# Kernel optimization log

Hardware: AMD Instinct MI355X
Metric: run time of the kernel (lower is better)

## Reference

```python
import jax, jax.numpy as jnp
import numpy as np

D_MODEL = 1024
B, T = 4, 2048
NEG = -1000000000.0


def setup_inputs() -> dict:
    key = jax.random.key(0)
    kq, kk, kv = jax.random.split(key, 3)
    query = jax.random.normal(kq, (B, T, D_MODEL), dtype=jnp.float32)
    k = jax.random.normal(kk, (B, T, D_MODEL), dtype=jnp.float32)
    value = jax.random.normal(kv, (B, T, D_MODEL), dtype=jnp.float32)
    # causal mask: 1.0 where attention is disallowed (strictly upper triangular)
    mask = jnp.triu(jnp.ones((T, T), dtype=jnp.float32), k=1)
    return {"query": query, "key": k, "value": value, "mask": mask}


def reference(query, key, value, mask):
    # dk = sqrt(1/d_model); logits = QK^T / dk  (i.e. * sqrt(d_model)) -- faithful to source
    dk = jnp.sqrt(jnp.float32(1.0) / jnp.float32(D_MODEL))
    attn_logits = jnp.einsum("btc,bsc->bts", query, key) / dk
    attn_logits = attn_logits + mask * NEG  # mask broadcasts over batch
    score = jax.nn.softmax(attn_logits, axis=-1)
    attention = jnp.einsum("bts,bsc->btc", score, value)
    return attention
```

## Files before the change

### kernel.cpp

```cpp
#include <hip/hip_runtime.h>

#define BB 4
#define TT 2048
#define DD 1024
#define SCALE 32.0f
#define NTILE 136
#define L2E 1.4426950408889634f

typedef _Float16 f16;
typedef __attribute__((ext_vector_type(4))) _Float16 half4v;
typedef __attribute__((ext_vector_type(8))) _Float16 half8v;
typedef __attribute__((ext_vector_type(16))) float f32x16;

typedef const __attribute__((address_space(1))) unsigned int* gas_u32;
typedef __attribute__((address_space(3))) unsigned int* las_u32;

static __device__ inline void gload16(const void* g, void* l) {
    __builtin_amdgcn_global_load_lds((gas_u32)g, (las_u32)l, 16, 0, 0);
}

static __device__ inline half8v ld_frag(const f16* p) {
    half4v a = *(const half4v*)p;
    half4v b = *(const half4v*)(p + 4);
    half8v r;
    r[0] = a[0]; r[1] = a[1]; r[2] = a[2]; r[3] = a[3];
    r[4] = b[0]; r[5] = b[1]; r[6] = b[2]; r[7] = b[3];
    return r;
}


__global__ __launch_bounds__(256) void repack_qk(const float* __restrict__ Q,
                                                 const float* __restrict__ K,
                                                 f16* __restrict__ Qt,
                                                 f16* __restrict__ Kt) {
    const int total = 2 * BB * TT * (DD / 8);
    for (int gid = blockIdx.x * 256 + threadIdx.x; gid < total; gid += gridDim.x * 256) {
        int g = gid & 127;
        int t = (gid >> 7) & 2047;
        int b = (gid >> 18) & 3;
        int which = gid >> 20;
        const float* src = which ? K : Q;
        f16* dst = which ? Kt : Qt;
        float sc = which ? 1.0f : SCALE;
        const float* p = src + ((size_t)(b * TT + t)) * DD + g * 8;
        float4 x0 = *(const float4*)p;
        float4 x1 = *(const float4*)(p + 4);
        float vv[8] = {x0.x, x0.y, x0.z, x0.w, x1.x, x1.y, x1.z, x1.w};
        half8v hi, lo;
#pragma unroll
        for (int e = 0; e < 8; ++e) {
            float x = vv[e] * sc;
            f16 h = (f16)x;
            hi[e] = h;
            lo[e] = (f16)(x - (float)h);
        }
        int r = t & 127, mi = t >> 7, ck = g >> 2, gq = g & 3;
        char* base = (char*)dst + ((size_t)((b * 16 + mi) * 32 + ck)) * 16384 + r * 128;
        *(half8v*)(base + ((gq ^ (r & 7)) << 4)) = hi;
        *(half8v*)(base + (((4 + gq) ^ (r & 7)) << 4)) = lo;
    }
}

__global__ __launch_bounds__(256) void transpose_v(const float* __restrict__ V,
                                                   f16* __restrict__ Vt) {
    __shared__ float Vs[64][129];
    int bid = blockIdx.x;
    int b = bid >> 8, kb = (bid >> 3) & 31, nj = bid & 7;
    const float* src = V + ((size_t)(b * TT + kb * 64)) * DD + nj * 128;
    int tid = threadIdx.x;
#pragma unroll
    for (int it = 0; it < 8; ++it) {
        int f4 = it * 256 + tid;
        int row = f4 >> 5, c4 = f4 & 31;
        float4 x = *(const float4*)(src + (size_t)row * DD + c4 * 4);
        Vs[row][c4 * 4 + 0] = x.x;
        Vs[row][c4 * 4 + 1] = x.y;
        Vs[row][c4 * 4 + 2] = x.z;
        Vs[row][c4 * 4 + 3] = x.w;
    }
    __syncthreads();
    char* dbase = (char*)Vt + ((size_t)((b * 8 + nj) * 32 + kb)) * 16384;
#pragma unroll
    for (int it = 0; it < 4; ++it) {
        int gid = it * 256 + tid;
        int n = gid >> 3, s = gid & 7;
        half8v h;
#pragma unroll
        for (int j = 0; j < 8; ++j) h[j] = (f16)Vs[s * 8 + j][n];
        *(half8v*)(dbase + n * 128 + ((s ^ (n & 7)) << 4)) = h;
    }
}

__global__ __launch_bounds__(256, 2) void k1_qk2(const f16* __restrict__ Qt,
                                                 const f16* __restrict__ Kt,
                                                 float* __restrict__ S) {
    __shared__ char lds[65536];

    int bid0 = blockIdx.x;
    int bid = (bid0 & 7) * (BB * NTILE / 8) + (bid0 >> 3);
    int b = bid / NTILE, r = bid % NTILE;
    int mi = 0;
    while ((mi + 1) * (mi + 2) / 2 <= r) ++mi;
    int nj = r - mi * (mi + 1) / 2;

    const char* Abase = (const char*)Qt + ((size_t)((b * 16 + mi) * 32)) * 16384;
    const char* Bbase = (const char*)Kt + ((size_t)((b * 16 + nj) * 32)) * 16384;
    float* Sb = S + (size_t)b * TT * TT + (size_t)(mi * 128) * TT + nj * 128;

    int tid = threadIdx.x;
    int lane = tid & 63;
    int wv = tid >> 6;
    int l31 = lane & 31, lhi = lane >> 5;
    int wrow = wv >> 1, wcol = wv & 1;

    int aoff[2][2], boff[2][2];
#pragma unroll
    for (int fm = 0; fm < 2; ++fm) {
        int ra = wrow * 64 + fm * 32 + l31;
        int rb = wcol * 64 + fm * 32 + l31;
#pragma unroll
        for (int ks = 0; ks < 2; ++ks) {
            int slot = ks * 2 + lhi;
            aoff[fm][ks] = ra * 128 + ((slot ^ (ra & 7)) << 4);
            boff[fm][ks] = rb * 128 + ((slot ^ (rb & 7)) << 4);
        }
    }
    int lane_go = (wv * 256 + lane) * 16;
    int lane_lo = (wv * 256) * 16;

    f32x16 acc[2][2] = {};

#define K1_STAGE(CK, BUF)                                                       \
    {                                                                           \
        const char* ga = Abase + (size_t)(CK) * 16384 + lane_go;                \
        const char* gb = Bbase + (size_t)(CK) * 16384 + lane_go;                \
        char* la = lds + (BUF) * 32768 + lane_lo;                               \
        char* lb = la + 16384;                                                  \
        _Pragma("unroll") for (int i = 0; i < 4; ++i)                           \
            gload16(ga + i * 1024, la + i * 1024);                              \
        _Pragma("unroll") for (int i = 0; i < 4; ++i)                           \
            gload16(gb + i * 1024, lb + i * 1024);                              \
    }

    K1_STAGE(0, 0);
    int cur = 0;
    for (int ck = 0; ck < 32; ++ck) {
        __syncthreads();
        if (ck + 1 < 32) K1_STAGE(ck + 1, cur ^ 1);
        const char* As = lds + cur * 32768;
        const char* Bs = As + 16384;
#pragma unroll
        for (int ks = 0; ks < 2; ++ks) {
            half8v ah[2], al[2], bh[2], bl[2];
#pragma unroll
            for (int f = 0; f < 2; ++f) {
                ah[f] = *(const half8v*)(As + aoff[f][ks]);
                al[f] = *(const half8v*)(As + (aoff[f][ks] ^ 64));
                bh[f] = *(const half8v*)(Bs + boff[f][ks]);
                bl[f] = *(const half8v*)(Bs + (boff[f][ks] ^ 64));
            }
#pragma unroll
            for (int fm = 0; fm < 2; ++fm)
#pragma unroll
                for (int fn = 0; fn < 2; ++fn) {
                    acc[fm][fn] = __builtin_amdgcn_mfma_f32_32x32x16_f16(ah[fm], bh[fn], acc[fm][fn], 0, 0, 0);
                    acc[fm][fn] = __builtin_amdgcn_mfma_f32_32x32x16_f16(ah[fm], bl[fn], acc[fm][fn], 0, 0, 0);
                    acc[fm][fn] = __builtin_amdgcn_mfma_f32_32x32x16_f16(al[fm], bh[fn], acc[fm][fn], 0, 0, 0);
                }
        }
        cur ^= 1;
    }
#pragma unroll
    for (int fm = 0; fm < 2; ++fm)
#pragma unroll
        for (int fn = 0; fn < 2; ++fn)
#pragma unroll
            for (int g = 0; g < 16; ++g) {
                int rr = (g & 3) + 8 * (g >> 2) + 4 * lhi;
                int row = wrow * 64 + fm * 32 + rr;
                int col = wcol * 64 + fn * 32 + l31;
                Sb[(size_t)row * TT + col] = acc[fm][fn][g];
            }
}

__global__ __launch_bounds__(256) void k1b2(const float* __restrict__ S,
                                            f16* __restrict__ Pt) {
    __shared__ float red[4];
    int rowid = blockIdx.x;
    int b = rowid >> 11, t = rowid & (TT - 1);
    const float* Sr = S + ((size_t)b * TT + t) * TT;
    int tid = threadIdx.x;
    int nv = t + 1;
    int mi = t >> 7, r = t & 127;
    int rowend = (mi + 1) << 7;
    int c = tid * 8;

    float4 x0 = *(const float4*)(Sr + c);
    float4 x1 = *(const float4*)(Sr + c + 4);
    float v[8] = {x0.x, x0.y, x0.z, x0.w, x1.x, x1.y, x1.z, x1.w};

    float m = -3.0e38f;
#pragma unroll
    for (int j = 0; j < 8; ++j)
        if (c + j < nv) m = fmaxf(m, v[j]);
#pragma unroll
    for (int o = 32; o > 0; o >>= 1) m = fmaxf(m, __shfl_xor(m, o));
    if ((tid & 63) == 0) red[tid >> 6] = m;
    __syncthreads();
    m = fmaxf(fmaxf(red[0], red[1]), fmaxf(red[2], red[3]));
    __syncthreads();

    float e[8];
    float s = 0.f;
#pragma unroll
    for (int j = 0; j < 8; ++j) {
        e[j] = (c + j < nv) ? exp2f((v[j] - m) * L2E) : 0.0f;
        s += e[j];
    }
#pragma unroll
    for (int o = 32; o > 0; o >>= 1) s += __shfl_xor(s, o);
    if ((tid & 63) == 0) red[tid >> 6] = s;
    __syncthreads();
    s = red[0] + red[1] + red[2] + red[3];
    float inv = 1.0f / s;

    if (c < rowend) {
        half8v h;
#pragma unroll
        for (int j = 0; j < 8; ++j) h[j] = (f16)(e[j] * inv);
        char* dst = (char*)Pt + ((size_t)((b * 16 + mi) * 32 + (c >> 6))) * 16384
                    + r * 128 + ((((c >> 3) & 7) ^ (r & 7)) << 4);
        *(half8v*)dst = h;
    }
}

__global__ __launch_bounds__(256, 2) void k2_pv2(const f16* __restrict__ Pt,
                                                 const f16* __restrict__ Vt,
                                                 float* __restrict__ O) {
    __shared__ char lds[65536];

    int bid0 = blockIdx.x;
    int bid = (bid0 & 7) * (512 / 8) + (bid0 >> 3);
    int b = bid >> 7, mi = (bid >> 3) & 15, nj = bid & 7;
    int kc = (mi + 1) * 2;

    const char* Abase = (const char*)Pt + ((size_t)((b * 16 + mi) * 32)) * 16384;
    const char* Bbase = (const char*)Vt + ((size_t)((b * 8 + nj) * 32)) * 16384;
    float* Ob = O + (size_t)b * TT * DD + (size_t)(mi * 128) * DD + nj * 128;

    int tid = threadIdx.x;
    int lane = tid & 63;
    int wv = tid >> 6;
    int l31 = lane & 31, lhi = lane >> 5;
    int wrow = wv >> 1, wcol = wv & 1;

    int aoff[2][4], boff[2][4];
#pragma unroll
    for (int f = 0; f < 2; ++f) {
        int ra = wrow * 64 + f * 32 + l31;
        int rb = wcol * 64 + f * 32 + l31;
#pragma unroll
        for (int ks = 0; ks < 4; ++ks) {
            int slot = ks * 2 + lhi;
            aoff[f][ks] = ra * 128 + ((slot ^ (ra & 7)) << 4);
            boff[f][ks] = rb * 128 + ((slot ^ (rb & 7)) << 4);
        }
    }
    int lane_go = (wv * 256 + lane) * 16;
    int lane_lo = (wv * 256) * 16;

    f32x16 acc[2][2] = {};

#define K2_STAGE(CK, BUF)                                                       \
    {                                                                           \
        const char* ga = Abase + (size_t)(CK) * 16384 + lane_go;                \
        const char* gb = Bbase + (size_t)(CK) * 16384 + lane_go;                \
        char* la = lds + (BUF) * 32768 + lane_lo;                               \
        char* lb = la + 16384;                                                  \
        _Pragma("unroll") for (int i = 0; i < 4; ++i)                           \
            gload16(ga + i * 1024, la + i * 1024);                              \
        _Pragma("unroll") for (int i = 0; i < 4; ++i)                           \
            gload16(gb + i * 1024, lb + i * 1024);                              \
    }

    K2_STAGE(0, 0);
    int cur = 0;
    for (int ck = 0; ck < kc; ++ck) {
        __syncthreads();
        if (ck + 1 < kc) K2_STAGE(ck + 1, cur ^ 1);
        const char* As = lds + cur * 32768;
        const char* Bs = As + 16384;
#pragma unroll
        for (int ks = 0; ks < 4; ++ks) {
            half8v a0 = *(const half8v*)(As + aoff[0][ks]);
            half8v a1 = *(const half8v*)(As + aoff[1][ks]);
            half8v b0 = *(const half8v*)(Bs + boff[0][ks]);
            half8v b1 = *(const half8v*)(Bs + boff[1][ks]);
            acc[0][0] = __builtin_amdgcn_mfma_f32_32x32x16_f16(a0, b0, acc[0][0], 0, 0, 0);
            acc[0][1] = __builtin_amdgcn_mfma_f32_32x32x16_f16(a0, b1, acc[0][1], 0, 0, 0);
            acc[1][0] = __builtin_amdgcn_mfma_f32_32x32x16_f16(a1, b0, acc[1][0], 0, 0, 0);
            acc[1][1] = __builtin_amdgcn_mfma_f32_32x32x16_f16(a1, b1, acc[1][1], 0, 0, 0);
        }
        cur ^= 1;
    }
#pragma unroll
    for (int fm = 0; fm < 2; ++fm)
#pragma unroll
        for (int fn = 0; fn < 2; ++fn)
#pragma unroll
            for (int g = 0; g < 16; ++g) {
                int rr = (g & 3) + 8 * (g >> 2) + 4 * lhi;
                int row = wrow * 64 + fm * 32 + rr;
                int col = wcol * 64 + fn * 32 + l31;
                Ob[(size_t)row * DD + col] = acc[fm][fn][g];
            }
}

__global__ __launch_bounds__(256, 2) void k1_qk(const float* __restrict__ Q,
                                                const float* __restrict__ Kmat,
                                                float* __restrict__ S) {
    __shared__ f16 Ah[128][36], Al[128][36], Bh[128][36], Bl[128][36];
    int bid = blockIdx.x;
    int b = bid / NTILE, r = bid % NTILE;
    int mi = 0;
    while ((mi + 1) * (mi + 2) / 2 <= r) ++mi;
    int nj = r - mi * (mi + 1) / 2;
    const float* Qb = Q + ((size_t)b * TT + (size_t)mi * 128) * DD;
    const float* Kb = Kmat + ((size_t)b * TT + (size_t)nj * 128) * DD;
    float* Sb = S + (size_t)b * TT * TT + (size_t)(mi * 128) * TT + nj * 128;
    int tid = threadIdx.x;
    int lane = tid & 63;
    int wave = tid >> 6;
    int l31 = lane & 31, lhi = lane >> 5;
    int wrow = wave >> 1, wcol = wave & 1;
    int r0 = tid >> 1;
    int c0 = (tid & 1) * 16;
    f32x16 acc[2][2] = {};
    float4 abuf[4], bbuf[4];
#pragma unroll
    for (int j = 0; j < 4; ++j) {
        abuf[j] = *(const float4*)(Qb + (size_t)r0 * DD + c0 + 4 * j);
        bbuf[j] = *(const float4*)(Kb + (size_t)r0 * DD + c0 + 4 * j);
    }
    for (int ch = 0; ch < DD / 32; ++ch) {
        __syncthreads();
#pragma unroll
        for (int j = 0; j < 4; ++j) {
            float4 a = abuf[j], bq = bbuf[j];
            float ax[4] = {a.x * SCALE, a.y * SCALE, a.z * SCALE, a.w * SCALE};
            float bx[4] = {bq.x, bq.y, bq.z, bq.w};
            half4v ahv, alv, bhv, blv;
#pragma unroll
            for (int e = 0; e < 4; ++e) {
                f16 h = (f16)ax[e];
                ahv[e] = h;
                alv[e] = (f16)(ax[e] - (float)h);
                f16 g = (f16)bx[e];
                bhv[e] = g;
                blv[e] = (f16)(bx[e] - (float)g);
            }
            *(half4v*)&Ah[r0][c0 + 4 * j] = ahv;
            *(half4v*)&Al[r0][c0 + 4 * j] = alv;
            *(half4v*)&Bh[r0][c0 + 4 * j] = bhv;
            *(half4v*)&Bl[r0][c0 + 4 * j] = blv;
        }
        __syncthreads();
        if (ch + 1 < DD / 32) {
            int ck = (ch + 1) * 32;
#pragma unroll
            for (int j = 0; j < 4; ++j) {
                abuf[j] = *(const float4*)(Qb + (size_t)r0 * DD + ck + c0 + 4 * j);
                bbuf[j] = *(const float4*)(Kb + (size_t)r0 * DD + ck + c0 + 4 * j);
            }
        }
#pragma unroll
        for (int ks = 0; ks < 2; ++ks) {
            int kb = ks * 16 + lhi * 8;
            half8v ahf[2], alf[2], bhf[2], blf[2];
#pragma unroll
            for (int f = 0; f < 2; ++f) {
                ahf[f] = ld_frag(&Ah[wrow * 64 + f * 32 + l31][kb]);
                alf[f] = ld_frag(&Al[wrow * 64 + f * 32 + l31][kb]);
                bhf[f] = ld_frag(&Bh[wcol * 64 + f * 32 + l31][kb]);
                blf[f] = ld_frag(&Bl[wcol * 64 + f * 32 + l31][kb]);
            }
#pragma unroll
            for (int fm = 0; fm < 2; ++fm)
#pragma unroll
                for (int fn = 0; fn < 2; ++fn) {
                    acc[fm][fn] = __builtin_amdgcn_mfma_f32_32x32x16_f16(ahf[fm], bhf[fn], acc[fm][fn], 0, 0, 0);
                    acc[fm][fn] = __builtin_amdgcn_mfma_f32_32x32x16_f16(ahf[fm], blf[fn], acc[fm][fn], 0, 0, 0);
                    acc[fm][fn] = __builtin_amdgcn_mfma_f32_32x32x16_f16(alf[fm], bhf[fn], acc[fm][fn], 0, 0, 0);
                }
        }
    }
#pragma unroll
    for (int fm = 0; fm < 2; ++fm)
#pragma unroll
        for (int fn = 0; fn < 2; ++fn)
#pragma unroll
            for (int g = 0; g < 16; ++g) {
                int rr = (g & 3) + 8 * (g >> 2) + 4 * lhi;
                int row = wrow * 64 + fm * 32 + rr;
                int col = wcol * 64 + fn * 32 + l31;
                Sb[(size_t)row * TT + col] = acc[fm][fn][g];
            }
}

__global__ __launch_bounds__(256) void k1b_softmax(const float* __restrict__ S,
                                                   f16* __restrict__ P) {
    __shared__ float red[4];
    int rowid = blockIdx.x;
    int b = rowid >> 11, t = rowid & (TT - 1);
    const float* Sr = S + (size_t)b * TT * TT + (size_t)t * TT;
    f16* Pr = P + (size_t)b * TT * TT + (size_t)t * TT;
    int tid = threadIdx.x;
    int nv = t + 1;
    int rowend = ((t >> 7) + 1) << 7;
    float m = -3.0e38f;
    for (int c = tid; c < nv; c += 256) m = fmaxf(m, Sr[c]);
#pragma unroll
    for (int o = 32; o > 0; o >>= 1) m = fmaxf(m, __shfl_xor(m, o));
    if ((tid & 63) == 0) red[tid >> 6] = m;
    __syncthreads();
    m = fmaxf(fmaxf(red[0], red[1]), fmaxf(red[2], red[3]));
    __syncthreads();
    float s = 0.f;
    for (int c = tid; c < nv; c += 256) s += exp2f((Sr[c] - m) * L2E);
#pragma unroll
    for (int o = 32; o > 0; o >>= 1) s += __shfl_xor(s, o);
    if ((tid & 63) == 0) red[tid >> 6] = s;
    __syncthreads();
    s = red[0] + red[1] + red[2] + red[3];
    float inv = 1.0f / s;
    for (int c = tid; c < rowend; c += 256) {
        float p = (c < nv) ? exp2f((Sr[c] - m) * L2E) * inv : 0.0f;
        Pr[c] = (f16)p;
    }
}

__global__ __launch_bounds__(256, 2) void k2_pv(const f16* __restrict__ P,
                                                const float* __restrict__ V,
                                                float* __restrict__ O) {
    __shared__ f16 Pa[128][36];
    __shared__ f16 Vt[128][36];
    int bid = blockIdx.x;
    int b = bid >> 7;
    int rest = bid & 127;
    int mi = rest >> 3, nj = rest & 7;
    int kend = (mi + 1) * 128;
    const f16* Pb = P + (size_t)b * TT * TT + (size_t)(mi * 128) * TT;
    const float* Vb = V + (size_t)b * TT * DD + nj * 128;
    float* Ob = O + (size_t)b * TT * DD + (size_t)(mi * 128) * DD + nj * 128;
    int tid = threadIdx.x;
    int lane = tid & 63;
    int wave = tid >> 6;
    int l31 = lane & 31, lhi = lane >> 5;
    int wrow = wave >> 1, wcol = wave & 1;
    f32x16 acc[2][2] = {};
    int pr = tid >> 1, pc = (tid & 1) * 16;
    int vk = tid >> 3, vn = (tid & 7) * 16;
    uint2 pbuf[4];
    float4 vbuf[4];
#pragma unroll
    for (int j = 0; j < 4; ++j) {
        pbuf[j] = *(const uint2*)(Pb + (size_t)pr * TT + pc + 4 * j);
        vbuf[j] = *(const float4*)(Vb + (size_t)vk * DD + vn + 4 * j);
    }
    for (int ck = 0; ck < kend; ck += 32) {
        __syncthreads();
#pragma unroll
        for (int j = 0; j < 4; ++j) {
            *(uint2*)&Pa[pr][pc + 4 * j] = pbuf[j];
            float4 v = vbuf[j];
            float vv[4] = {v.x, v.y, v.z, v.w};
            int n0 = vn + 4 * j;
#pragma unroll
            for (int e = 0; e < 4; ++e) {
                int n = n0 + e;
                Vt[n][vk ^ ((((unsigned)n >> 4) & 3) << 3)] = (f16)vv[e];
            }
        }
        __syncthreads();
        if (ck + 32 < kend) {
            int cn = ck + 32;
#pragma unroll
            for (int j = 0; j < 4; ++j) {
                pbuf[j] = *(const uint2*)(Pb + (size_t)pr * TT + cn + pc + 4 * j);
                vbuf[j] = *(const float4*)(Vb + (size_t)(cn + vk) * DD + vn + 4 * j);
            }
        }
#pragma unroll
        for (int ks = 0; ks < 2; ++ks) {
            int kb = ks * 16 + lhi * 8;
            half8v paf[2], vbf[2];
#pragma unroll
            for (int f = 0; f < 2; ++f) {
                paf[f] = ld_frag(&Pa[wrow * 64 + f * 32 + l31][kb]);
                int n = wcol * 64 + f * 32 + l31;
                int kbs = kb ^ ((((unsigned)n >> 4) & 3) << 3);
                vbf[f] = ld_frag(&Vt[n][kbs]);
            }
#pragma unroll
            for (int fm = 0; fm < 2; ++fm)
#pragma unroll
                for (int fn = 0; fn < 2; ++fn)
                    acc[fm][fn] = __builtin_amdgcn_mfma_f32_32x32x16_f16(paf[fm], vbf[fn], acc[fm][fn], 0, 0, 0);
        }
    }
#pragma unroll
    for (int fm = 0; fm < 2; ++fm)
#pragma unroll
        for (int fn = 0; fn < 2; ++fn)
#pragma unroll
            for (int g = 0; g < 16; ++g) {
                int rr = (g & 3) + 8 * (g >> 2) + 4 * lhi;
                int row = wrow * 64 + fm * 32 + rr;
                int col = wcol * 64 + fn * 32 + l31;
                Ob[(size_t)row * DD + col] = acc[fm][fn][g];
            }
}

__global__ __launch_bounds__(256) void fa_fallback(const float* __restrict__ Q,
                                                   const float* __restrict__ Kmat,
                                                   const float* __restrict__ V,
                                                   float* __restrict__ O) {
    __shared__ float qs[DD];
    __shared__ float osum[DD];
    __shared__ float red[4];
    int rowid = blockIdx.x;
    int b = rowid >> 11, t = rowid & (TT - 1);
    const float* q = Q + ((size_t)b * TT + t) * DD;
    int tid = threadIdx.x;
    for (int j = tid; j < DD; j += 256) { qs[j] = q[j] * SCALE; osum[j] = 0.f; }
    __syncthreads();
    float m = -3.0e38f, l = 0.f;
    for (int s = 0; s <= t; ++s) {
        const float* kr = Kmat + ((size_t)b * TT + s) * DD;
        float part = 0.f;
#pragma unroll
        for (int j = 0; j < 4; ++j) part += qs[tid * 4 + j] * kr[tid * 4 + j];
#pragma unroll
        for (int o = 32; o > 0; o >>= 1) part += __shfl_xor(part, o);
        if ((tid & 63) == 0) red[tid >> 6] = part;
        __syncthreads();
        float dot = red[0] + red[1] + red[2] + red[3];
        float mn = fmaxf(m, dot);
        float f = exp2f((m - mn) * 1.44269504f);
        float e = exp2f((dot - mn) * 1.44269504f);
        l = l * f + e;
        const float* vr = V + ((size_t)b * TT + s) * DD;
#pragma unroll
        for (int j = 0; j < 4; ++j) {
            int c = tid * 4 + j;
            osum[c] = osum[c] * f + e * vr[c];
        }
        m = mn;
        __syncthreads();
    }
    float inv = 1.f / l;
    for (int j = tid; j < DD; j += 256) O[((size_t)b * TT + t) * DD + j] = osum[j] * inv;
}

extern "C" void kernel_launch(void* const* d_in, const int* in_sizes, int n_in,
                              void* d_out, int out_size, void* d_ws, size_t ws_size,
                              hipStream_t stream) {
    const float* Q = (const float*)d_in[0];
    const float* K = (const float*)d_in[1];
    const float* V = (const float*)d_in[2];
    float* O = (float*)d_out;

    const size_t MB = 1024 * 1024;
    const size_t QT_B = 32 * MB, KT_B = 32 * MB, VT_B = 16 * MB, S_B = 64 * MB;
    const size_t FULL = QT_B + KT_B + VT_B + S_B;

    size_t sbytes = (size_t)BB * TT * TT * 4;
    size_t pbytes = (size_t)BB * TT * TT * 2;

    if (ws_size >= FULL) {
        f16* Qt = (f16*)d_ws;
        f16* Kt = (f16*)((char*)d_ws + QT_B);
        f16* Vt = (f16*)((char*)d_ws + QT_B + KT_B);
        float* S = (float*)((char*)d_ws + QT_B + KT_B + VT_B);
        f16* Pt = (f16*)d_ws;
        hipLaunchKernelGGL(repack_qk, dim3(2048), dim3(256), 0, stream, Q, K, Qt, Kt);
        hipLaunchKernelGGL(transpose_v, dim3(1024), dim3(256), 0, stream, V, Vt);
        hipLaunchKernelGGL(k1_qk2, dim3(BB * NTILE), dim3(256), 0, stream, Qt, Kt, S);
        hipLaunchKernelGGL(k1b2, dim3(BB * TT), dim3(256), 0, stream, S, Pt);
        hipLaunchKernelGGL(k2_pv2, dim3(512), dim3(256), 0, stream, Pt, Vt, O);
    } else if (ws_size >= sbytes + pbytes) {
        float* S = (float*)d_ws;
        f16* P = (f16*)((char*)d_ws + sbytes);
        hipLaunchKernelGGL(k1_qk, dim3(BB * NTILE), dim3(256), 0, stream, Q, K, S);
        hipLaunchKernelGGL(k1b_softmax, dim3(BB * TT), dim3(256), 0, stream, S, P);
        hipLaunchKernelGGL(k2_pv, dim3(BB * 16 * 8), dim3(256), 0, stream, P, V, O);
    } else {
        hipLaunchKernelGGL(fa_fallback, dim3(BB * TT), dim3(256), 0, stream, Q, K, V, O);
    }
}
```

Before: 153.7 us.

## Switch to slot-major 8KB chunk layout, widen PV tiles, skip masked softmax loads

The repacked Q/K/V/P buffers move from 16KB swizzled chunks to 8KB slot-major chunks, so each fragment row is contiguous and needs no XOR swizzle. QK uses half the LDS per block with occupancy raised to 3, and the PV kernel computes 128x256 output tiles with 256 blocks, reusing each P tile across two V column blocks. Repack_qk now stages through shared memory to write coalesced 128-byte rows, and softmax skips loading S entries beyond the causal tile. The unswizzled LDS layout may cause bank conflicts, and halving the PV grid reduces parallelism on a large GPU.

```diff
diff --git a/kernel.cpp b/kernel.cpp
--- a/kernel.cpp
+++ b/kernel.cpp
@@ -33,32 +33,39 @@
                                                  const float* __restrict__ K,
                                                  f16* __restrict__ Qt,
                                                  f16* __restrict__ Kt) {
-    const int total = 2 * BB * TT * (DD / 8);
-    for (int gid = blockIdx.x * 256 + threadIdx.x; gid < total; gid += gridDim.x * 256) {
-        int g = gid & 127;
-        int t = (gid >> 7) & 2047;
-        int b = (gid >> 18) & 3;
-        int which = gid >> 20;
-        const float* src = which ? K : Q;
-        f16* dst = which ? Kt : Qt;
-        float sc = which ? 1.0f : SCALE;
-        const float* p = src + ((size_t)(b * TT + t)) * DD + g * 8;
-        float4 x0 = *(const float4*)p;
-        float4 x1 = *(const float4*)(p + 4);
+    __shared__ char rl[32768];
+    int bid = blockIdx.x;
+    int which = bid >> 10, b = (bid >> 8) & 3, mi = (bid >> 4) & 15, ks4 = bid & 15;
+    const float* src = which ? K : Q;
+    f16* dst = which ? Kt : Qt;
+    float sc = which ? 1.0f : SCALE;
+
+    int tid = threadIdx.x;
+    int r = tid >> 1, h = tid & 1;
+    const float* p = src + ((size_t)(b * TT + mi * 128 + r)) * DD + ks4 * 64 + h * 32;
+#pragma unroll
+    for (int j = 0; j < 4; ++j) {
+        float4 x0 = *(const float4*)(p + j * 8);
+        float4 x1 = *(const float4*)(p + j * 8 + 4);
         float vv[8] = {x0.x, x0.y, x0.z, x0.w, x1.x, x1.y, x1.z, x1.w};
         half8v hi, lo;
 #pragma unroll
         for (int e = 0; e < 8; ++e) {
             float x = vv[e] * sc;
-            f16 h = (f16)x;
-            hi[e] = h;
-            lo[e] = (f16)(x - (float)h);
-        }
-        int r = t & 127, mi = t >> 7, ck = g >> 2, gq = g & 3;
-        char* base = (char*)dst + ((size_t)((b * 16 + mi) * 32 + ck)) * 16384 + r * 128;
-        *(half8v*)(base + ((gq ^ (r & 7)) << 4)) = hi;
-        *(half8v*)(base + (((4 + gq) ^ (r & 7)) << 4)) = lo;
-    }
+            f16 hh = (f16)x;
+            hi[e] = hh;
+            lo[e] = (f16)(x - (float)hh);
+        }
+        int ckl = h * 2 + (j >> 1);
+        int shalf = j & 1;
+        *(half8v*)(rl + ckl * 8192 + shalf * 2048 + r * 16) = hi;
+        *(half8v*)(rl + ckl * 8192 + (2 + shalf) * 2048 + r * 16) = lo;
+    }
+    __syncthreads();
+    char* gout = (char*)dst + ((size_t)((b * 16 + mi) * 64 + ks4 * 4)) * 8192 + tid * 128;
+#pragma unroll
+    for (int q = 0; q < 8; ++q)
+        *(float4*)(gout + q * 16) = *(float4*)(rl + tid * 128 + q * 16);
 }
 
 __global__ __launch_bounds__(256) void transpose_v(const float* __restrict__ V,
@@ -79,32 +86,33 @@
         Vs[row][c4 * 4 + 3] = x.w;
     }
     __syncthreads();
-    char* dbase = (char*)Vt + ((size_t)((b * 8 + nj) * 32 + kb)) * 16384;
-#pragma unroll
-    for (int it = 0; it < 4; ++it) {
-        int gid = it * 256 + tid;
-        int n = gid >> 3, s = gid & 7;
-        half8v h;
-#pragma unroll
-        for (int j = 0; j < 8; ++j) h[j] = (f16)Vs[s * 8 + j][n];
-        *(half8v*)(dbase + n * 128 + ((s ^ (n & 7)) << 4)) = h;
-    }
-}
-
-__global__ __launch_bounds__(256, 2) void k1_qk2(const f16* __restrict__ Qt,
+#pragma unroll
+    for (int qq = 0; qq < 4; ++qq) {
+        int q = tid * 4 + qq;
+        int ckl = q >> 9, s = (q >> 7) & 3, n = q & 127;
+        half8v hv;
+#pragma unroll
+        for (int e = 0; e < 8; ++e) hv[e] = (f16)Vs[ckl * 32 + s * 8 + e][n];
+        char* out = (char*)Vt + ((size_t)((b * 8 + nj) * 64 + kb * 2 + ckl)) * 8192
+                    + s * 2048 + n * 16;
+        *(half8v*)out = hv;
+    }
+}
+
+__global__ __launch_bounds__(256, 3) void k1_qk3(const f16* __restrict__ Qt,
                                                  const f16* __restrict__ Kt,
                                                  float* __restrict__ S) {
-    __shared__ char lds[65536];
+    __shared__ char lds[32768];
 
     int bid0 = blockIdx.x;
     int bid = (bid0 & 7) * (BB * NTILE / 8) + (bid0 >> 3);
-    int b = bid / NTILE, r = bid % NTILE;
+    int b = bid / NTILE, rr0 = bid % NTILE;
     int mi = 0;
-    while ((mi + 1) * (mi + 2) / 2 <= r) ++mi;
-    int nj = r - mi * (mi + 1) / 2;
-
-    const char* Abase = (const char*)Qt + ((size_t)((b * 16 + mi) * 32)) * 16384;
-    const char* Bbase = (const char*)Kt + ((size_t)((b * 16 + nj) * 32)) * 16384;
+    while ((mi + 1) * (mi + 2) / 2 <= rr0) ++mi;
+    int nj = rr0 - mi * (mi + 1) / 2;
+
+    const char* Abase = (const char*)Qt + ((size_t)((b * 16 + mi) * 64)) * 8192;
+    const char* Bbase = (const char*)Kt + ((size_t)((b * 16 + nj) * 64)) * 8192;
     float* Sb = S + (size_t)b * TT * TT + (size_t)(mi * 128) * TT + nj * 128;
 
     int tid = threadIdx.x;
@@ -113,63 +121,57 @@
     int l31 = lane & 31, lhi = lane >> 5;
     int wrow = wv >> 1, wcol = wv & 1;
 
-    int aoff[2][2], boff[2][2];
-#pragma unroll
-    for (int fm = 0; fm < 2; ++fm) {
-        int ra = wrow * 64 + fm * 32 + l31;
-        int rb = wcol * 64 + fm * 32 + l31;
-#pragma unroll
-        for (int ks = 0; ks < 2; ++ks) {
-            int slot = ks * 2 + lhi;
-            aoff[fm][ks] = ra * 128 + ((slot ^ (ra & 7)) << 4);
-            boff[fm][ks] = rb * 128 + ((slot ^ (rb & 7)) << 4);
-        }
-    }
-    int lane_go = (wv * 256 + lane) * 16;
-    int lane_lo = (wv * 256) * 16;
+    int aoff[2], boff[2];
+#pragma unroll
+    for (int f = 0; f < 2; ++f) {
+        int ra = wrow * 64 + f * 32 + l31;
+        int rb = wcol * 64 + f * 32 + l31;
+        aoff[f] = lhi * 2048 + ra * 16;
+        boff[f] = lhi * 2048 + rb * 16;
+    }
+    int lane_go = wv * 2048 + lane * 16;
+    int lane_lo = wv * 2048;
 
     f32x16 acc[2][2] = {};
 
 #define K1_STAGE(CK, BUF)                                                       \
     {                                                                           \
-        const char* ga = Abase + (size_t)(CK) * 16384 + lane_go;                \
-        const char* gb = Bbase + (size_t)(CK) * 16384 + lane_go;                \
-        char* la = lds + (BUF) * 32768 + lane_lo;                               \
-        char* lb = la + 16384;                                                  \
-        _Pragma("unroll") for (int i = 0; i < 4; ++i)                           \
-            gload16(ga + i * 1024, la + i * 1024);                              \
-        _Pragma("unroll") for (int i = 0; i < 4; ++i)                           \
-            gload16(gb + i * 1024, lb + i * 1024);                              \
+        const char* ga = Abase + (size_t)(CK) * 8192 + lane_go;                 \
+        const char* gb = Bbase + (size_t)(CK) * 8192 + lane_go;                 \
+        char* la = lds + (BUF) * 16384 + lane_lo;                               \
+        char* lb = la + 8192;                                                   \
+        gload16(ga, la);                                                        \
+        gload16(ga + 1024, la + 1024);                                          \
+        gload16(gb, lb);                                                        \
+        gload16(gb + 1024, lb + 1024);                                          \
     }
 
     K1_STAGE(0, 0);
     int cur = 0;
-    for (int ck = 0; ck < 32; ++ck) {
-        __syncthreads();
-        if (ck + 1 < 32) K1_STAGE(ck + 1, cur ^ 1);
-        const char* As = lds + cur * 32768;
-        const char* Bs = As + 16384;
-#pragma unroll
-        for (int ks = 0; ks < 2; ++ks) {
-            half8v ah[2], al[2], bh[2], bl[2];
-#pragma unroll
-            for (int f = 0; f < 2; ++f) {
-                ah[f] = *(const half8v*)(As + aoff[f][ks]);
-                al[f] = *(const half8v*)(As + (aoff[f][ks] ^ 64));
-                bh[f] = *(const half8v*)(Bs + boff[f][ks]);
-                bl[f] = *(const half8v*)(Bs + (boff[f][ks] ^ 64));
-            }
-#pragma unroll
-            for (int fm = 0; fm < 2; ++fm)
-#pragma unroll
-                for (int fn = 0; fn < 2; ++fn) {
-                    acc[fm][fn] = __builtin_amdgcn_mfma_f32_32x32x16_f16(ah[fm], bh[fn], acc[fm][fn], 0, 0, 0);
-                    acc[fm][fn] = __builtin_amdgcn_mfma_f32_32x32x16_f16(ah[fm], bl[fn], acc[fm][fn], 0, 0, 0);
-                    acc[fm][fn] = __builtin_amdgcn_mfma_f32_32x32x16_f16(al[fm], bh[fn], acc[fm][fn], 0, 0, 0);
-                }
-        }
+    for (int ck = 0; ck < 64; ++ck) {
+        __syncthreads();
+        if (ck + 1 < 64) K1_STAGE(ck + 1, cur ^ 1);
+        const char* As = lds + cur * 16384;
+        const char* Bs = As + 8192;
+        half8v ah[2], al[2], bh[2], bl[2];
+#pragma unroll
+        for (int f = 0; f < 2; ++f) {
+            ah[f] = *(const half8v*)(As + aoff[f]);
+            al[f] = *(const half8v*)(As + aoff[f] + 4096);
+            bh[f] = *(const half8v*)(Bs + boff[f]);
+            bl[f] = *(const half8v*)(Bs + boff[f] + 4096);
+        }
+#pragma unroll
+        for (int fm = 0; fm < 2; ++fm)
+#pragma unroll
+            for (int fn = 0; fn < 2; ++fn) {
+                acc[fm][fn] = __builtin_amdgcn_mfma_f32_32x32x16_f16(ah[fm], bh[fn], acc[fm][fn], 0, 0, 0);
+                acc[fm][fn] = __builtin_amdgcn_mfma_f32_32x32x16_f16(ah[fm], bl[fn], acc[fm][fn], 0, 0, 0);
+                acc[fm][fn] = __builtin_amdgcn_mfma_f32_32x32x16_f16(al[fm], bh[fn], acc[fm][fn], 0, 0, 0);
+            }
         cur ^= 1;
     }
+#undef K1_STAGE
 #pragma unroll
     for (int fm = 0; fm < 2; ++fm)
 #pragma unroll
@@ -183,7 +185,7 @@
             }
 }
 
-__global__ __launch_bounds__(256) void k1b2(const float* __restrict__ S,
+__global__ __launch_bounds__(256) void k1b3(const float* __restrict__ S,
                                             f16* __restrict__ Pt) {
     __shared__ float red[4];
     int rowid = blockIdx.x;
@@ -194,15 +196,22 @@
     int mi = t >> 7, r = t & 127;
     int rowend = (mi + 1) << 7;
     int c = tid * 8;
-
-    float4 x0 = *(const float4*)(Sr + c);
-    float4 x1 = *(const float4*)(Sr + c + 4);
-    float v[8] = {x0.x, x0.y, x0.z, x0.w, x1.x, x1.y, x1.z, x1.w};
+    bool act = c < rowend;
+
+    float v[8] = {0, 0, 0, 0, 0, 0, 0, 0};
+    if (act) {
+        float4 x0 = *(const float4*)(Sr + c);
+        float4 x1 = *(const float4*)(Sr + c + 4);
+        v[0] = x0.x; v[1] = x0.y; v[2] = x0.z; v[3] = x0.w;
+        v[4] = x1.x; v[5] = x1.y; v[6] = x1.z; v[7] = x1.w;
+    }
 
     float m = -3.0e38f;
-#pragma unroll
-    for (int j = 0; j < 8; ++j)
-        if (c + j < nv) m = fmaxf(m, v[j]);
+    if (act) {
+#pragma unroll
+        for (int j = 0; j < 8; ++j)
+            if (c + j < nv) m = fmaxf(m, v[j]);
+    }
 #pragma unroll
     for (int o = 32; o > 0; o >>= 1) m = fmaxf(m, __shfl_xor(m, o));
     if ((tid & 63) == 0) red[tid >> 6] = m;
@@ -214,7 +223,7 @@
     float s = 0.f;
 #pragma unroll
     for (int j = 0; j < 8; ++j) {
-        e[j] = (c + j < nv) ? exp2f((v[j] - m) * L2E) : 0.0f;
+        e[j] = (act && c + j < nv) ? exp2f((v[j] - m) * L2E) : 0.0f;
         s += e[j];
     }
 #pragma unroll
@@ -224,63 +233,52 @@
     s = red[0] + red[1] + red[2] + red[3];
     float inv = 1.0f / s;
 
-    if (c < rowend) {
-        half8v h;
-#pragma unroll
-        for (int j = 0; j < 8; ++j) h[j] = (f16)(e[j] * inv);
-        char* dst = (char*)Pt + ((size_t)((b * 16 + mi) * 32 + (c >> 6))) * 16384
-                    + r * 128 + ((((c >> 3) & 7) ^ (r & 7)) << 4);
-        *(half8v*)dst = h;
-    }
-}
-
-__global__ __launch_bounds__(256, 2) void k2_pv2(const f16* __restrict__ Pt,
+    if (act) {
+        half8v hv;
+#pragma unroll
+        for (int j = 0; j < 8; ++j) hv[j] = (f16)(e[j] * inv);
+        int ck = c >> 5, sl = (c >> 3) & 3;
+        char* dst = (char*)Pt + ((size_t)((b * 16 + mi) * 64 + ck)) * 8192
+                    + sl * 2048 + r * 16;
+        *(half8v*)dst = hv;
+    }
+}
+
+__global__ __launch_bounds__(256, 2) void k2_pv3(const f16* __restrict__ Pt,
                                                  const f16* __restrict__ Vt,
                                                  float* __restrict__ O) {
-    __shared__ char lds[65536];
+    __shared__ char lds[49152];
 
     int bid0 = blockIdx.x;
-    int bid = (bid0 & 7) * (512 / 8) + (bid0 >> 3);
-    int b = bid >> 7, mi = (bid >> 3) & 15, nj = bid & 7;
-    int kc = (mi + 1) * 2;
-
-    const char* Abase = (const char*)Pt + ((size_t)((b * 16 + mi) * 32)) * 16384;
-    const char* Bbase = (const char*)Vt + ((size_t)((b * 8 + nj) * 32)) * 16384;
-    float* Ob = O + (size_t)b * TT * DD + (size_t)(mi * 128) * DD + nj * 128;
+    int bid = (bid0 & 7) * 32 + (bid0 >> 3);
+    int b = bid >> 6, mi = (bid >> 2) & 15, nj2 = bid & 3;
+    int kc = (mi + 1) * 4;
+
+    const char* Abase = (const char*)Pt + ((size_t)((b * 16 + mi) * 64)) * 8192;
+    const char* B0base = (const char*)Vt + ((size_t)((b * 8 + nj2 * 2) * 64)) * 8192;
+    const char* B1base = (const char*)Vt + ((size_t)((b * 8 + nj2 * 2 + 1) * 64)) * 8192;
+    float* Ob = O + (size_t)b * TT * DD + (size_t)(mi * 128) * DD + nj2 * 256;
 
     int tid = threadIdx.x;
     int lane = tid & 63;
     int wv = tid >> 6;
     int l31 = lane & 31, lhi = lane >> 5;
-    int wrow = wv >> 1, wcol = wv & 1;
-
-    int aoff[2][4], boff[2][4];
-#pragma unroll
-    for (int f = 0; f < 2; ++f) {
-        int ra = wrow * 64 + f * 32 + l31;
-        int rb = wcol * 64 + f * 32 + l31;
-#pragma unroll
-        for (int ks = 0; ks < 4; ++ks) {
-            int slot = ks * 2 + lhi;
-            aoff[f][ks] = ra * 128 + ((slot ^ (ra & 7)) << 4);
-            boff[f][ks] = rb * 128 + ((slot ^ (rb & 7)) << 4);
-        }
-    }
-    int lane_go = (wv * 256 + lane) * 16;
-    int lane_lo = (wv * 256) * 16;
-
-    f32x16 acc[2][2] = {};
+    int wr = wv >> 1, wc = wv & 1;
+
+    f32x16 acc[2][4] = {};
+    int lane16 = lane * 16;
 
 #define K2_STAGE(CK, BUF)                                                       \
     {                                                                           \
-        const char* ga = Abase + (size_t)(CK) * 16384 + lane_go;                \
-        const char* gb = Bbase + (size_t)(CK) * 16384 + lane_go;                \
-        char* la = lds + (BUF) * 32768 + lane_lo;                               \
-        char* lb = la + 16384;                                                  \
-        _Pragma("unroll") for (int i = 0; i < 4; ++i)                           \
-            gload16(ga + i * 1024, la + i * 1024);                              \
-        _Pragma("unroll") for (int i = 0; i < 4; ++i)                           \
-            gload16(gb + i * 1024, lb + i * 1024);                              \
+        size_t gck = (size_t)(CK) * 8192;                                       \
+        char* lb = lds + (BUF) * 24576;                                         \
+        _Pragma("unroll") for (int i = 0; i < 6; ++i) {                         \
+            int off = (i * 4 + wv) * 1024;                                      \
+            const char* gsrc = (off < 8192) ? (Abase + gck + off)               \
+                             : (off < 16384) ? (B0base + gck + off - 8192)      \
+                                             : (B1base + gck + off - 16384);    \
+            gload16(gsrc + lane16, lb + off);                                   \
+        }                                                                       \
     }
 
     K2_STAGE(0, 0);
@@ -288,30 +286,38 @@
     for (int ck = 0; ck < kc; ++ck) {
         __syncthreads();
         if (ck + 1 < kc) K2_STAGE(ck + 1, cur ^ 1);
-        const char* As = lds + cur * 32768;
-        const char* Bs = As + 16384;
-#pragma unroll
-        for (int ks = 0; ks < 4; ++ks) {
-            half8v a0 = *(const half8v*)(As + aoff[0][ks]);
-            half8v a1 = *(const half8v*)(As + aoff[1][ks]);
-            half8v b0 = *(const half8v*)(Bs + boff[0][ks]);
-            half8v b1 = *(const half8v*)(Bs + boff[1][ks]);
+        const char* As = lds + cur * 24576;
+        const char* Bs = As + 8192 + wc * 8192;
+#pragma unroll
+        for (int ks = 0; ks < 2; ++ks) {
+            int slot = (ks * 2 + lhi) * 2048;
+            half8v a0 = *(const half8v*)(As + slot + (wr * 64 + l31) * 16);
+            half8v a1 = *(const half8v*)(As + slot + (wr * 64 + 32 + l31) * 16);
+            half8v b0 = *(const half8v*)(Bs + slot + (l31) * 16);
+            half8v b1 = *(const half8v*)(Bs + slot + (32 + l31) * 16);
+            half8v b2 = *(const half8v*)(Bs + slot + (64 + l31) * 16);
+            half8v b3 = *(const half8v*)(Bs + slot + (96 + l31) * 16);
             acc[0][0] = __builtin_amdgcn_mfma_f32_32x32x16_f16(a0, b0, acc[0][0], 0, 0, 0);
             acc[0][1] = __builtin_amdgcn_mfma_f32_32x32x16_f16(a0, b1, acc[0][1], 0, 0, 0);
+            acc[0][2] = __builtin_amdgcn_mfma_f32_32x32x16_f16(a0, b2, acc[0][2], 0, 0, 0);
+            acc[0][3] = __builtin_amdgcn_mfma_f32_32x32x16_f16(a0, b3, acc[0][3], 0, 0, 0);
             acc[1][0] = __builtin_amdgcn_mfma_f32_32x32x16_f16(a1, b0, acc[1][0], 0, 0, 0);
             acc[1][1] = __builtin_amdgcn_mfma_f32_32x32x16_f16(a1, b1, acc[1][1], 0, 0, 0);
+            acc[1][2] = __builtin_amdgcn_mfma_f32_32x32x16_f16(a1, b2, acc[1][2], 0, 0, 0);
+            acc[1][3] = __builtin_amdgcn_mfma_f32_32x32x16_f16(a1, b3, acc[1][3], 0, 0, 0);
         }
         cur ^= 1;
     }
+#undef K2_STAGE
 #pragma unroll
     for (int fm = 0; fm < 2; ++fm)
 #pragma unroll
-        for (int fn = 0; fn < 2; ++fn)
+        for (int fn = 0; fn < 4; ++fn)
 #pragma unroll
             for (int g = 0; g < 16; ++g) {
                 int rr = (g & 3) + 8 * (g >> 2) + 4 * lhi;
-                int row = wrow * 64 + fm * 32 + rr;
-                int col = wcol * 64 + fn * 32 + l31;
+                int row = wr * 64 + fm * 32 + rr;
+                int col = wc * 128 + fn * 32 + l31;
                 Ob[(size_t)row * DD + col] = acc[fm][fn][g];
             }
 }
@@ -443,7 +449,7 @@
                                                 const float* __restrict__ V,
                                                 float* __restrict__ O) {
     __shared__ f16 Pa[128][36];
-    __shared__ f16 Vt[128][36];
+    __shared__ f16 Vtt[128][36];
     int bid = blockIdx.x;
     int b = bid >> 7;
     int rest = bid & 127;
@@ -478,7 +484,7 @@
 #pragma unroll
             for (int e = 0; e < 4; ++e) {
                 int n = n0 + e;
-                Vt[n][vk ^ ((((unsigned)n >> 4) & 3) << 3)] = (f16)vv[e];
+                Vtt[n][vk ^ ((((unsigned)n >> 4) & 3) << 3)] = (f16)vv[e];
             }
         }
         __syncthreads();
@@ -499,7 +505,7 @@
                 paf[f] = ld_frag(&Pa[wrow * 64 + f * 32 + l31][kb]);
                 int n = wcol * 64 + f * 32 + l31;
                 int kbs = kb ^ ((((unsigned)n >> 4) & 3) << 3);
-                vbf[f] = ld_frag(&Vt[n][kbs]);
+                vbf[f] = ld_frag(&Vtt[n][kbs]);
             }
 #pragma unroll
             for (int fm = 0; fm < 2; ++fm)
@@ -585,9 +591,9 @@
         f16* Pt = (f16*)d_ws;
         hipLaunchKernelGGL(repack_qk, dim3(2048), dim3(256), 0, stream, Q, K, Qt, Kt);
         hipLaunchKernelGGL(transpose_v, dim3(1024), dim3(256), 0, stream, V, Vt);
-        hipLaunchKernelGGL(k1_qk2, dim3(BB * NTILE), dim3(256), 0, stream, Qt, Kt, S);
-        hipLaunchKernelGGL(k1b2, dim3(BB * TT), dim3(256), 0, stream, S, Pt);
-        hipLaunchKernelGGL(k2_pv2, dim3(512), dim3(256), 0, stream, Pt, Vt, O);
+        hipLaunchKernelGGL(k1_qk3, dim3(BB * NTILE), dim3(256), 0, stream, Qt, Kt, S);
+        hipLaunchKernelGGL(k1b3, dim3(BB * TT), dim3(256), 0, stream, S, Pt);
+        hipLaunchKernelGGL(k2_pv3, dim3(256), dim3(256), 0, stream, Pt, Vt, O);
     } else if (ws_size >= sbytes + pbytes) {
         float* S = (float*)d_ws;
         f16* P = (f16*)((char*)d_ws + sbytes);
```

Measured after the change: 171.6 us. +11.7%, slower.
